# Optimization experiments

Measured on AMD Instinct MI355X. Metric: run time of the kernel, lower is better.

Reference implementation:

```python
import jax, jax.numpy as jnp
import numpy as np

D = 128      # dim_hidden
L = 8        # topological levels (level 0 = primary inputs)
M = 32768    # nodes per level
N = L * M
G = 5        # gate types: maj/not/and/or/xor -> 5 param sets
F = 2        # fan-in per gate node


def setup_inputs() -> dict:
    key = jax.random.key(0)
    ks = jax.random.split(key, 18)
    p = lambda k, sh: jax.random.normal(k, sh, jnp.float32) * 0.05
    return {
        's': jax.random.normal(ks[0], (N, D), jnp.float32),
        't': jax.random.normal(ks[1], (N, D), jnp.float32),
        'gate': jax.random.randint(ks[2], (N,), 0, G, jnp.int32),
        'fanin': jax.random.randint(ks[3], (L - 1, M, F), 0, M, jnp.int32),
        'hs_W': p(ks[4], (2 * D, D)), 'hs_b': p(ks[5], (D,)),
        'aggr_W1': p(ks[6], (G, 2 * D, D)), 'aggr_b1': p(ks[7], (G, D)),
        'aggr_W2': p(ks[8], (G, D, D)), 'aggr_b2': p(ks[9], (G, D)),
        'aggr_W3': p(ks[10], (G, D, D)), 'aggr_b3': p(ks[11], (G, D)),
        'gru_Wi': p(ks[12], (G, D, 3 * D)), 'gru_Wh': p(ks[13], (G, D, 3 * D)),
        'gru_bi': p(ks[14], (G, 3 * D)), 'gru_bh': p(ks[15], (G, 3 * D)),
    }


def _forward(s, t, gate, fanin, hs_W, hs_b, aggr_W1, aggr_b1, aggr_W2, aggr_b2,
             aggr_W3, aggr_b3, gru_Wi, gru_Wh, gru_bi, gru_bh):
    hs = jnp.concatenate([s, t], -1) @ hs_W + hs_b          # [N,D]
    hf = jnp.zeros((N, D), hs.dtype)                        # functional state, zero-init
    for lvl in range(1, L):                                 # level-synchronous sweep
        lo = lvl * M
        g_l = gate[lo:lo + M]                               # [M] gate type of dst nodes
        oh = jax.nn.one_hot(g_l, G, dtype=hs.dtype)         # [M,G] gate selector
        src = (lvl - 1) * M + fanin[lvl - 1]                # [M,F] global fan-in indices
        src_state = jnp.concatenate([hs[src], hf[src]], -1)  # [M,F,2D] node_state gather
        # per-gate-type edge MLP (TFMlpAggr): 3-layer MLP on source states, sum over fan-in
        h1 = jax.nn.relu(jnp.einsum('mfc,gcd->gmfd', src_state, aggr_W1) + aggr_b1[:, None, None, :])
        h2 = jax.nn.relu(jnp.einsum('gmfd,gde->gmfe', h1, aggr_W2) + aggr_b2[:, None, None, :])
        m = jnp.einsum('gmfe,gek->gmfk', h2, aggr_W3) + aggr_b3[:, None, None, :]
        msg = jnp.einsum('gmd,mg->md', m.sum(axis=2), oh)   # [M,D] select own gate's aggr
        # per-gate-type GRU update of hf (torch GRU math, seq_len=1)
        h = hf[lo:lo + M]                                   # [M,D]
        gi = jnp.einsum('md,gdk->gmk', msg, gru_Wi) + gru_bi[:, None, :]  # [G,M,3D]
        gh = jnp.einsum('md,gdk->gmk', h, gru_Wh) + gru_bh[:, None, :]
        r = jax.nn.sigmoid(gi[..., :D] + gh[..., :D])
        z = jax.nn.sigmoid(gi[..., D:2 * D] + gh[..., D:2 * D])
        n = jnp.tanh(gi[..., 2 * D:] + r * gh[..., 2 * D:])
        h_new = jnp.einsum('gmd,mg->md', (1.0 - z) * n + z * h[None], oh)
        hf = hf.at[lo:lo + M].set(h_new)                    # scatter-write back
    return hs, hf


def reference(s, t, gate, fanin, hs_W, hs_b, aggr_W1, aggr_b1, aggr_W2, aggr_b2,
              aggr_W3, aggr_b3, gru_Wi, gru_Wh, gru_bi, gru_bh):
    return _forward(s, t, gate, fanin, hs_W, hs_b, aggr_W1, aggr_b1, aggr_W2,
                    aggr_b2, aggr_W3, aggr_b3, gru_Wi, gru_Wh, gru_bi, gru_bh)
```

## Files before the change

kernel.cpp:

```cpp
#include <hip/hip_runtime.h>
#include <hip/hip_bf16.h>

#define DD 128
#define LL 8
#define MM 32768
#define NN (LL*MM)
#define GG 5
#define FF 2
#define SORT_STRIDE 33408

typedef __attribute__((ext_vector_type(8))) short short8;
typedef __attribute__((ext_vector_type(4))) short short4v;
typedef __attribute__((ext_vector_type(4))) float f32x4;

#define MFMA16(a,b,c) __builtin_amdgcn_mfma_f32_16x16x32_bf16((a),(b),(c),0,0,0)

__device__ __forceinline__ short f2bf(float x){
  __hip_bfloat16 h = __float2bfloat16(x);
  return *reinterpret_cast<short*>(&h);
}

__device__ __forceinline__ short8 pack8(f32x4 a, f32x4 b){
  short8 r;
  r[0]=f2bf(a[0]); r[1]=f2bf(a[1]); r[2]=f2bf(a[2]); r[3]=f2bf(a[3]);
  r[4]=f2bf(b[0]); r[5]=f2bf(b[1]); r[6]=f2bf(b[2]); r[7]=f2bf(b[3]);
  return r;
}

__global__ void prep_kernel(const float* __restrict__ hs_W, const float* __restrict__ W1,
                            const float* __restrict__ W2, const float* __restrict__ W3,
                            const float* __restrict__ Wi,
                            short* __restrict__ hsWt, short* __restrict__ W1t,
                            short* __restrict__ W2t, short* __restrict__ W3t,
                            short* __restrict__ Wit, int* __restrict__ cntcur)
{
  if (blockIdx.x == 0 && threadIdx.x < 70) cntcur[threadIdx.x] = 0;
  int u = blockIdx.x*256 + threadIdx.x;
  const float* src; short* dst; int ldw;
  if (u < 4096){
    int i=u, ct=i>>9, kc=(i>>6)&7, lane=i&63;
    src = hs_W + (size_t)(kc*32 + 8*(lane>>4))*128 + ct*16 + (lane&15);
    dst = hsWt + (size_t)i*8; ldw=128;
  } else if (u < 24576){
    int v=u-4096, g=v>>12, i=v&4095, ct=i>>9, kc=(i>>6)&7, lane=i&63;
    src = W1 + (size_t)g*32768 + (size_t)(kc*32 + 8*(lane>>4))*128 + ct*16 + (lane&15);
    dst = W1t + (size_t)g*32768 + i*8; ldw=128;
  } else if (u < 34816){
    int v=u-24576, g=v>>11, i=v&2047, ct=i>>8, kc=(i>>6)&3, lane=i&63;
    src = W2 + (size_t)g*16384 + (size_t)(kc*32 + 8*(lane>>4))*128 + ct*16 + (lane&15);
    dst = W2t + (size_t)g*16384 + i*8; ldw=128;
  } else if (u < 45056){
    int v=u-34816, g=v>>11, i=v&2047, ct=i>>8, kc=(i>>6)&3, lane=i&63;
    src = W3 + (size_t)g*16384 + (size_t)(kc*32 + 8*(lane>>4))*128 + ct*16 + (lane&15);
    dst = W3t + (size_t)g*16384 + i*8; ldw=128;
  } else {
    int v=u-45056, g=v/6144, i=v%6144, ct=i>>8, kc=(i>>6)&3, lane=i&63;
    src = Wi + (size_t)g*49152 + (size_t)(kc*32 + 8*(lane>>4))*384 + ct*16 + (lane&15);
    dst = Wit + (size_t)g*49152 + i*8; ldw=384;
  }
  short8 o;
#pragma unroll
  for (int j=0;j<8;++j) o[j] = f2bf(src[(size_t)j*ldw]);
  *(short8*)dst = o;
}

__global__ void count_kernel(const int* __restrict__ gate, int* __restrict__ cnt){
  __shared__ int lc[GG];
  const int li = blockIdx.x >> 7;
  const int m  = ((blockIdx.x & 127) << 8) + threadIdx.x;
  if (threadIdx.x < GG) lc[threadIdx.x] = 0;
  __syncthreads();
  int g = gate[(li+1)*MM + m];
  atomicAdd(&lc[g], 1);
  __syncthreads();
  if (threadIdx.x < GG && lc[threadIdx.x] > 0)
    atomicAdd(&cnt[li*GG + threadIdx.x], lc[threadIdx.x]);
}

__global__ void offs_kernel(const int* __restrict__ cnt, int* __restrict__ off,
                            int* __restrict__ pend, int* __restrict__ sorted){
  __shared__ int se[35], sp[35];
  const int tid = threadIdx.x;
  if (tid < LL-1){
    int l = tid, o = 0;
    for (int g = 0; g < GG; ++g){
      off[l*GG+g] = o;
      int c = cnt[l*GG+g];
      pend[l*GG+g] = o + c;
      se[l*GG+g] = o + c;
      o += ((c + 127) >> 7) << 7;
      sp[l*GG+g] = o;
    }
  }
  __syncthreads();
  for (int b = 0; b < 35; ++b){
    int l = b / GG;
    for (int i = se[b] + tid; i < sp[b]; i += 256)
      sorted[l*SORT_STRIDE + i] = -1;
  }
}

__global__ void scatter_kernel(const int* __restrict__ gate, const int* __restrict__ off,
                               int* __restrict__ cur, int* __restrict__ sorted){
  __shared__ int lc[GG];
  __shared__ int base[GG];
  const int li = blockIdx.x >> 7;
  const int m  = ((blockIdx.x & 127) << 8) + threadIdx.x;
  if (threadIdx.x < GG) lc[threadIdx.x] = 0;
  __syncthreads();
  int g = gate[(li+1)*MM + m];
  int p = atomicAdd(&lc[g], 1);
  __syncthreads();
  if (threadIdx.x < GG)
    base[threadIdx.x] = atomicAdd(&cur[li*GG + threadIdx.x], lc[threadIdx.x]);
  __syncthreads();
  sorted[li*SORT_STRIDE + off[li*GG+g] + base[g] + p] = m;
}

__global__ __launch_bounds__(512,4) void hs_kernel(
    const float* __restrict__ s, const float* __restrict__ t,
    const short* __restrict__ Wt, const float* __restrict__ b,
    float* __restrict__ hs, short* __restrict__ hs_sh,
    float* __restrict__ hf, short* __restrict__ hf_sh)
{
  __shared__ __align__(16) short Xs[32768];
  const int tid=threadIdx.x, lane=tid&63, w=tid>>6;
  const int l15=lane&15, lq=lane>>4;
  const int wr=w>>2, wc=w&3;
  const int row0 = blockIdx.x*128;

  {
    const int r = tid>>2, p = tid&3;
    const float* srow = s + (size_t)(row0+r)*DD;
    const float* trow = t + (size_t)(row0+r)*DD;
    const int rf = r>>4, rl = r&15;
#pragma unroll
    for (int i=0;i<8;++i){
      int u = p + 4*i;
      const float* pp = (u<16) ? (srow + 8*u) : (trow + 8*(u-16));
      short8 v = pack8(*(const f32x4*)pp, *(const f32x4*)(pp+4));
      *(short8*)(Xs + ((rf*8+(u>>2))*64 + (u&3)*16 + rl)*8) = v;
    }
  }

  if (row0 < MM){
    f32x4 zf4 = {0.f,0.f,0.f,0.f};
    short8 zs8 = {0,0,0,0,0,0,0,0};
    const size_t basei = (size_t)row0*DD;
    for (int i=tid; i<4096; i+=512) *(f32x4*)(hf + basei + i*4) = zf4;
    for (int i=tid; i<2048; i+=512) *(short8*)(hf_sh + basei + i*8) = zs8;
  }
  __syncthreads();

  f32x4 zf = {0.f,0.f,0.f,0.f};
  f32x4 acc[4][2];
#pragma unroll
  for (int rr=0;rr<4;++rr){ acc[rr][0]=zf; acc[rr][1]=zf; }

  const short* Ab = Wt + lane*8;
#pragma unroll
  for (int kc=0;kc<8;++kc){
    short8 a0 = *(const short8*)(Ab + (16*wc + kc)*512);
    short8 a1 = *(const short8*)(Ab + (16*wc + 8 + kc)*512);
#pragma unroll
    for (int rr=0;rr<4;++rr){
      short8 bx = *(const short8*)(Xs + (((4*wr+rr)*8 + kc)*64 + lane)*8);
      acc[rr][0] = MFMA16(a0, bx, acc[rr][0]);
      acc[rr][1] = MFMA16(a1, bx, acc[rr][1]);
    }
  }

  f32x4 bv0 = *(const f32x4*)(b + 32*wc + 4*lq);
  f32x4 bv1 = *(const f32x4*)(b + 32*wc + 16 + 4*lq);
#pragma unroll
  for (int rr=0;rr<4;++rr){
    int row = row0 + (4*wr+rr)*16 + l15;
#pragma unroll
    for (int q=0;q<2;++q){
      f32x4 bv = q ? bv1 : bv0;
      int col = 32*wc + 16*q + 4*lq;
      f32x4 o; short4v pk;
#pragma unroll
      for (int j=0;j<4;++j){ o[j] = acc[rr][q][j] + bv[j]; pk[j] = f2bf(o[j]); }
      *(f32x4*)(hs + (size_t)row*DD + col) = o;
      *(short4v*)(hs_sh + (size_t)row*DD + col) = pk;
    }
  }
}

__global__ __launch_bounds__(512,4) void level_kernel(
    int lvl, float* __restrict__ hfg,
    const short* __restrict__ hs_sh, short* __restrict__ hf_sh,
    const int* __restrict__ fanin,
    const short* __restrict__ W1t, const short* __restrict__ W2t,
    const short* __restrict__ W3t, const short* __restrict__ Wit,
    const float* __restrict__ b1, const float* __restrict__ b2,
    const float* __restrict__ b3, const float* __restrict__ bi,
    const float* __restrict__ bh,
    const int* __restrict__ off, const int* __restrict__ pend,
    const int* __restrict__ sorted)
{
  __shared__ __align__(16) short Xs[32768];
  __shared__ int nodebuf[64];
  __shared__ int srcbuf[128];
  __shared__ int ginfo;

  const int tid=threadIdx.x, lane=tid&63, w=tid>>6;
  const int l15=lane&15, lq=lane>>4;
  const int wr=w>>2, wc=w&3;
  const int li = lvl-1;
  const int pos0 = blockIdx.x*64;

  if (tid==0){
    int g=-1;
    for (int q=0;q<GG;++q)
      if (pos0>=off[li*GG+q] && pos0<pend[li*GG+q]){ g=q; break; }
    ginfo=g;
  }
  if (tid<64) nodebuf[tid] = sorted[li*SORT_STRIDE + pos0 + tid];
  if (tid<128){
    int mg = sorted[li*SORT_STRIDE + pos0 + (tid>>1)];
    srcbuf[tid] = (mg>=0) ? li*MM + fanin[((size_t)li*MM+mg)*FF + (tid&1)] : 0;
  }
  __syncthreads();
  const int g = ginfo;
  if (g<0) return;

  {
    const int r = tid>>2, p = tid&3;
    const int src = srcbuf[r];
    const short* hsrow = hs_sh + (size_t)src*DD;
    const short* hfrow = hf_sh + (size_t)src*DD;
    const int rf = r>>4, rl = r&15;
#pragma unroll
    for (int i=0;i<8;++i){
      int u = p + 4*i;
      short8 v = *(const short8*)((u<16) ? (hsrow + 8*u) : (hfrow + 8*(u-16)));
      *(short8*)(Xs + ((rf*8+(u>>2))*64 + (u&3)*16 + rl)*8) = v;
    }
  }
  __syncthreads();

  f32x4 zf = {0.f,0.f,0.f,0.f};

  f32x4 acc[4][2];
#pragma unroll
  for (int rr=0;rr<4;++rr){ acc[rr][0]=zf; acc[rr][1]=zf; }
  const short* A1 = W1t + (size_t)g*32768 + lane*8;
#pragma unroll
  for (int kc=0;kc<8;++kc){
    short8 a0 = *(const short8*)(A1 + (16*wc + kc)*512);
    short8 a1 = *(const short8*)(A1 + (16*wc + 8 + kc)*512);
#pragma unroll
    for (int rr=0;rr<4;++rr){
      short8 bx = *(const short8*)(Xs + (((4*wr+rr)*8 + kc)*64 + lane)*8);
      acc[rr][0] = MFMA16(a0, bx, acc[rr][0]);
      acc[rr][1] = MFMA16(a1, bx, acc[rr][1]);
    }
  }
  __syncthreads();
  {
    f32x4 bv0 = *(const f32x4*)(b1 + g*DD + 32*wc + 4*lq);
    f32x4 bv1 = *(const f32x4*)(b1 + g*DD + 32*wc + 16 + 4*lq);
#pragma unroll
    for (int rr=0;rr<4;++rr){
      int rf = 4*wr + rr;
#pragma unroll
      for (int q=0;q<2;++q){
        f32x4 bv = q ? bv1 : bv0;
        short4v pk;
#pragma unroll
        for (int j=0;j<4;++j) pk[j] = f2bf(fmaxf(acc[rr][q][j] + bv[j], 0.f));
        *(short4v*)(Xs + ((rf*4 + wc)*64 + (2*q + (lq>>1))*16 + l15)*8 + 4*(lq&1)) = pk;
      }
    }
  }
  __syncthreads();

  f32x4 acc2[4][2];
#pragma unroll
  for (int rr=0;rr<4;++rr){ acc2[rr][0]=zf; acc2[rr][1]=zf; }
  const short* A2 = W2t + (size_t)g*16384 + lane*8;
#pragma unroll
  for (int kc=0;kc<4;++kc){
    short8 a0 = *(const short8*)(A2 + (8*wc + kc)*512);
    short8 a1 = *(const short8*)(A2 + (8*wc + 4 + kc)*512);
#pragma unroll
    for (int rr=0;rr<4;++rr){
      short8 bx = *(const short8*)(Xs + (((4*wr+rr)*4 + kc)*64 + lane)*8);
      acc2[rr][0] = MFMA16(a0, bx, acc2[rr][0]);
      acc2[rr][1] = MFMA16(a1, bx, acc2[rr][1]);
    }
  }
  {
    f32x4 bv0 = *(const f32x4*)(b2 + g*DD + 32*wc + 4*lq);
    f32x4 bv1 = *(const f32x4*)(b2 + g*DD + 32*wc + 16 + 4*lq);
#pragma unroll
    for (int rr=0;rr<4;++rr){
      int rf = 4*wr + rr;
#pragma unroll
      for (int q=0;q<2;++q){
        f32x4 bv = q ? bv1 : bv0;
        short4v pk;
#pragma unroll
        for (int j=0;j<4;++j) pk[j] = f2bf(fmaxf(acc2[rr][q][j] + bv[j], 0.f));
        *(short4v*)(Xs + 16384 + ((rf*4 + wc)*64 + (2*q + (lq>>1))*16 + l15)*8 + 4*(lq&1)) = pk;
      }
    }
  }
  __syncthreads();

  f32x4 acc3[4][2];
#pragma unroll
  for (int rr=0;rr<4;++rr){ acc3[rr][0]=zf; acc3[rr][1]=zf; }
  const short* A3 = W3t + (size_t)g*16384 + lane*8;
#pragma unroll
  for (int kc=0;kc<4;++kc){
    short8 a0 = *(const short8*)(A3 + (8*wc + kc)*512);
    short8 a1 = *(const short8*)(A3 + (8*wc + 4 + kc)*512);
#pragma unroll
    for (int rr=0;rr<4;++rr){
      short8 bx = *(const short8*)(Xs + 16384 + (((4*wr+rr)*4 + kc)*64 + lane)*8);
      acc3[rr][0] = MFMA16(a0, bx, acc3[rr][0]);
      acc3[rr][1] = MFMA16(a1, bx, acc3[rr][1]);
    }
  }
  {
    f32x4 bv0 = *(const f32x4*)(b3 + g*DD + 32*wc + 4*lq);
    f32x4 bv1 = *(const f32x4*)(b3 + g*DD + 32*wc + 16 + 4*lq);
#pragma unroll
    for (int rr=0;rr<4;++rr){
#pragma unroll
      for (int q=0;q<2;++q){
        f32x4 bv = q ? bv1 : bv0;
        f32x4 mv;
#pragma unroll
        for (int j=0;j<4;++j){
          float v = acc3[rr][q][j];
          mv[j] = v + __shfl_xor(v, 1) + 2.f*bv[j];
        }
        if ((l15 & 1) == 0){
          int n = (4*wr+rr)*8 + (l15>>1);
          short4v pk;
#pragma unroll
          for (int j=0;j<4;++j) pk[j] = f2bf(mv[j]);
          *(short4v*)(Xs + (((n>>4)*4 + wc)*64 + (2*q + (lq>>1))*16 + (n&15))*8 + 4*(lq&1)) = pk;
        }
      }
    }
  }
  __syncthreads();

  f32x4 gr[4], gz[4], gn[4];
#pragma unroll
  for (int rfm=0;rfm<4;++rfm){ gr[rfm]=zf; gz[rfm]=zf; gn[rfm]=zf; }
  const short* AW = Wit + (size_t)g*49152 + lane*8;
#pragma unroll
  for (int kc=0;kc<4;++kc){
    short8 aR = *(const short8*)(AW + ((w)*4 + kc)*512);
    short8 aZ = *(const short8*)(AW + ((8+w)*4 + kc)*512);
    short8 aN = *(const short8*)(AW + ((16+w)*4 + kc)*512);
#pragma unroll
    for (int rfm=0;rfm<4;++rfm){
      short8 bm = *(const short8*)(Xs + ((rfm*4 + kc)*64 + lane)*8);
      gr[rfm] = MFMA16(aR, bm, gr[rfm]);
      gz[rfm] = MFMA16(aZ, bm, gz[rfm]);
      gn[rfm] = MFMA16(aN, bm, gn[rfm]);
    }
  }

  const int lo = lvl*MM;
  f32x4 biR = *(const f32x4*)(bi + g*384 + 16*w + 4*lq);
  f32x4 biZ = *(const f32x4*)(bi + g*384 + 128 + 16*w + 4*lq);
  f32x4 biN = *(const f32x4*)(bi + g*384 + 256 + 16*w + 4*lq);
  f32x4 bhR = *(const f32x4*)(bh + g*384 + 16*w + 4*lq);
  f32x4 bhZ = *(const f32x4*)(bh + g*384 + 128 + 16*w + 4*lq);
  f32x4 bhN = *(const f32x4*)(bh + g*384 + 256 + 16*w + 4*lq);
#pragma unroll
  for (int rfm=0;rfm<4;++rfm){
    int m = nodebuf[rfm*16 + l15];
    if (m < 0) continue;
    f32x4 o; short4v pk;
#pragma unroll
    for (int j=0;j<4;++j){
      float xr = gr[rfm][j] + biR[j] + bhR[j];
      float xz = gz[rfm][j] + biZ[j] + bhZ[j];
      float r_ = 1.f/(1.f + __expf(-xr));
      float z_ = 1.f/(1.f + __expf(-xz));
      float xn = gn[rfm][j] + biN[j] + r_*bhN[j];
      float n_ = 2.f/(1.f + __expf(-2.f*xn)) - 1.f;
      o[j] = (1.f - z_)*n_;
      pk[j] = f2bf(o[j]);
    }
    int col = 16*w + 4*lq;
    *(f32x4*)(hfg + (size_t)(lo + m)*DD + col) = o;
    *(short4v*)(hf_sh + (size_t)(lo + m)*DD + col) = pk;
  }
}

extern "C" void kernel_launch(void* const* d_in, const int* in_sizes, int n_in,
                              void* d_out, int out_size, void* d_ws, size_t ws_size,
                              hipStream_t stream)
{
  const float* s    = (const float*)d_in[0];
  const float* t    = (const float*)d_in[1];
  const int*   gate = (const int*)d_in[2];
  const int*   fanin= (const int*)d_in[3];
  const float* hs_W = (const float*)d_in[4];
  const float* hs_b = (const float*)d_in[5];
  const float* W1   = (const float*)d_in[6];
  const float* b1   = (const float*)d_in[7];
  const float* W2   = (const float*)d_in[8];
  const float* b2   = (const float*)d_in[9];
  const float* W3   = (const float*)d_in[10];
  const float* b3   = (const float*)d_in[11];
  const float* Wi   = (const float*)d_in[12];
  const float* bi   = (const float*)d_in[14];
  const float* bh   = (const float*)d_in[15];

  float* hs = (float*)d_out;
  float* hf = hs + (size_t)NN*DD;

  int* cnt    = (int*)d_ws;
  int* cur    = cnt + 35;
  int* off    = cnt + 70;
  int* pendv  = cnt + 105;
  int* sorted = cnt + 256;

  short* wbase = (short*)((char*)d_ws + (1<<20));
  short* hsWt = wbase;
  short* W1t  = wbase + 32768;
  short* W2t  = wbase + 196608;
  short* W3t  = wbase + 278528;
  short* Wit  = wbase + 360448;

  short* hs_sh = (short*)((char*)d_ws + (size_t)(8<<20));
  short* hf_sh = hs_sh + (size_t)NN*DD;

  prep_kernel<<<296, 256, 0, stream>>>(hs_W, W1, W2, W3, Wi,
                                       hsWt, W1t, W2t, W3t, Wit, cnt);
  count_kernel<<<896, 256, 0, stream>>>(gate, cnt);
  offs_kernel<<<1, 256, 0, stream>>>(cnt, off, pendv, sorted);
  scatter_kernel<<<896, 256, 0, stream>>>(gate, off, cur, sorted);
  hs_kernel<<<NN/128, 512, 0, stream>>>(s, t, hsWt, hs_b, hs, hs_sh, hf, hf_sh);
  for (int lvl = 1; lvl < LL; ++lvl){
    level_kernel<<<SORT_STRIDE/64, 512, 0, stream>>>(lvl, hf,
        hs_sh, hf_sh, fanin, W1t, W2t, W3t, Wit,
        b1, b2, b3, bi, bh, off, pendv, sorted);
  }
}
```

Measured before the change: 414.1 us.

## Halve level-kernel tile to 32 nodes with 256 threads and finer gate padding

Each level-kernel block now handles 32 destination nodes with 4 waves instead of 64 nodes with 8 waves. Shared memory is halved and the per-wave MFMA mapping is rearranged so each wave owns a 32-column slice for every GEMM, including the GRU stage. Per-gate bucket padding drops from 128 to 32, which wastes fewer padded rows across the 5 gate types and gives more blocks. In exchange, each weight fragment loaded from global memory is reused over fewer rows, so weight traffic per node roughly doubles.

```diff
diff --git a/kernel.cpp b/kernel.cpp
--- a/kernel.cpp
+++ b/kernel.cpp
@@ -88,7 +88,7 @@
       int c = cnt[l*GG+g];
       pend[l*GG+g] = o + c;
       se[l*GG+g] = o + c;
-      o += ((c + 127) >> 7) << 7;
+      o += ((c + 31) >> 5) << 5;
       sp[l*GG+g] = o;
     }
   }
@@ -188,7 +188,7 @@
   }
 }
 
-__global__ __launch_bounds__(512,4) void level_kernel(
+__global__ __launch_bounds__(256,4) void level_kernel(
     int lvl, float* __restrict__ hfg,
     const short* __restrict__ hs_sh, short* __restrict__ hf_sh,
     const int* __restrict__ fanin,
@@ -200,16 +200,15 @@
     const int* __restrict__ off, const int* __restrict__ pend,
     const int* __restrict__ sorted)
 {
-  __shared__ __align__(16) short Xs[32768];
-  __shared__ int nodebuf[64];
-  __shared__ int srcbuf[128];
+  __shared__ __align__(16) short Xs[16384];
+  __shared__ int nodebuf[32];
+  __shared__ int srcbuf[64];
   __shared__ int ginfo;
 
   const int tid=threadIdx.x, lane=tid&63, w=tid>>6;
   const int l15=lane&15, lq=lane>>4;
-  const int wr=w>>2, wc=w&3;
   const int li = lvl-1;
-  const int pos0 = blockIdx.x*64;
+  const int pos0 = blockIdx.x*32;
 
   if (tid==0){
     int g=-1;
@@ -217,8 +216,8 @@
       if (pos0>=off[li*GG+q] && pos0<pend[li*GG+q]){ g=q; break; }
     ginfo=g;
   }
-  if (tid<64) nodebuf[tid] = sorted[li*SORT_STRIDE + pos0 + tid];
-  if (tid<128){
+  if (tid<32) nodebuf[tid] = sorted[li*SORT_STRIDE + pos0 + tid];
+  if (tid<64){
     int mg = sorted[li*SORT_STRIDE + pos0 + (tid>>1)];
     srcbuf[tid] = (mg>=0) ? li*MM + fanin[((size_t)li*MM+mg)*FF + (tid&1)] : 0;
   }
@@ -249,29 +248,28 @@
   const short* A1 = W1t + (size_t)g*32768 + lane*8;
 #pragma unroll
   for (int kc=0;kc<8;++kc){
-    short8 a0 = *(const short8*)(A1 + (16*wc + kc)*512);
-    short8 a1 = *(const short8*)(A1 + (16*wc + 8 + kc)*512);
-#pragma unroll
-    for (int rr=0;rr<4;++rr){
-      short8 bx = *(const short8*)(Xs + (((4*wr+rr)*8 + kc)*64 + lane)*8);
+    short8 a0 = *(const short8*)(A1 + (16*w + kc)*512);
+    short8 a1 = *(const short8*)(A1 + (16*w + 8 + kc)*512);
+#pragma unroll
+    for (int rr=0;rr<4;++rr){
+      short8 bx = *(const short8*)(Xs + ((rr*8 + kc)*64 + lane)*8);
       acc[rr][0] = MFMA16(a0, bx, acc[rr][0]);
       acc[rr][1] = MFMA16(a1, bx, acc[rr][1]);
     }
   }
   __syncthreads();
   {
-    f32x4 bv0 = *(const f32x4*)(b1 + g*DD + 32*wc + 4*lq);
-    f32x4 bv1 = *(const f32x4*)(b1 + g*DD + 32*wc + 16 + 4*lq);
-#pragma unroll
-    for (int rr=0;rr<4;++rr){
-      int rf = 4*wr + rr;
+    f32x4 bv0 = *(const f32x4*)(b1 + g*DD + 32*w + 4*lq);
+    f32x4 bv1 = *(const f32x4*)(b1 + g*DD + 32*w + 16 + 4*lq);
+#pragma unroll
+    for (int rr=0;rr<4;++rr){
 #pragma unroll
       for (int q=0;q<2;++q){
         f32x4 bv = q ? bv1 : bv0;
         short4v pk;
 #pragma unroll
         for (int j=0;j<4;++j) pk[j] = f2bf(fmaxf(acc[rr][q][j] + bv[j], 0.f));
-        *(short4v*)(Xs + ((rf*4 + wc)*64 + (2*q + (lq>>1))*16 + l15)*8 + 4*(lq&1)) = pk;
+        *(short4v*)(Xs + ((rr*4 + w)*64 + (2*q + (lq>>1))*16 + l15)*8 + 4*(lq&1)) = pk;
       }
     }
   }
@@ -283,28 +281,27 @@
   const short* A2 = W2t + (size_t)g*16384 + lane*8;
 #pragma unroll
   for (int kc=0;kc<4;++kc){
-    short8 a0 = *(const short8*)(A2 + (8*wc + kc)*512);
-    short8 a1 = *(const short8*)(A2 + (8*wc + 4 + kc)*512);
-#pragma unroll
-    for (int rr=0;rr<4;++rr){
-      short8 bx = *(const short8*)(Xs + (((4*wr+rr)*4 + kc)*64 + lane)*8);
+    short8 a0 = *(const short8*)(A2 + (8*w + kc)*512);
+    short8 a1 = *(const short8*)(A2 + (8*w + 4 + kc)*512);
+#pragma unroll
+    for (int rr=0;rr<4;++rr){
+      short8 bx = *(const short8*)(Xs + ((rr*4 + kc)*64 + lane)*8);
       acc2[rr][0] = MFMA16(a0, bx, acc2[rr][0]);
       acc2[rr][1] = MFMA16(a1, bx, acc2[rr][1]);
     }
   }
   {
-    f32x4 bv0 = *(const f32x4*)(b2 + g*DD + 32*wc + 4*lq);
-    f32x4 bv1 = *(const f32x4*)(b2 + g*DD + 32*wc + 16 + 4*lq);
-#pragma unroll
-    for (int rr=0;rr<4;++rr){
-      int rf = 4*wr + rr;
+    f32x4 bv0 = *(const f32x4*)(b2 + g*DD + 32*w + 4*lq);
+    f32x4 bv1 = *(const f32x4*)(b2 + g*DD + 32*w + 16 + 4*lq);
+#pragma unroll
+    for (int rr=0;rr<4;++rr){
 #pragma unroll
       for (int q=0;q<2;++q){
         f32x4 bv = q ? bv1 : bv0;
         short4v pk;
 #pragma unroll
         for (int j=0;j<4;++j) pk[j] = f2bf(fmaxf(acc2[rr][q][j] + bv[j], 0.f));
-        *(short4v*)(Xs + 16384 + ((rf*4 + wc)*64 + (2*q + (lq>>1))*16 + l15)*8 + 4*(lq&1)) = pk;
+        *(short4v*)(Xs + 8192 + ((rr*4 + w)*64 + (2*q + (lq>>1))*16 + l15)*8 + 4*(lq&1)) = pk;
       }
     }
   }
@@ -316,18 +313,18 @@
   const short* A3 = W3t + (size_t)g*16384 + lane*8;
 #pragma unroll
   for (int kc=0;kc<4;++kc){
-    short8 a0 = *(const short8*)(A3 + (8*wc + kc)*512);
-    short8 a1 = *(const short8*)(A3 + (8*wc + 4 + kc)*512);
-#pragma unroll
-    for (int rr=0;rr<4;++rr){
-      short8 bx = *(const short8*)(Xs + 16384 + (((4*wr+rr)*4 + kc)*64 + lane)*8);
+    short8 a0 = *(const short8*)(A3 + (8*w + kc)*512);
+    short8 a1 = *(const short8*)(A3 + (8*w + 4 + kc)*512);
+#pragma unroll
+    for (int rr=0;rr<4;++rr){
+      short8 bx = *(const short8*)(Xs + 8192 + ((rr*4 + kc)*64 + lane)*8);
       acc3[rr][0] = MFMA16(a0, bx, acc3[rr][0]);
       acc3[rr][1] = MFMA16(a1, bx, acc3[rr][1]);
     }
   }
   {
-    f32x4 bv0 = *(const f32x4*)(b3 + g*DD + 32*wc + 4*lq);
-    f32x4 bv1 = *(const f32x4*)(b3 + g*DD + 32*wc + 16 + 4*lq);
+    f32x4 bv0 = *(const f32x4*)(b3 + g*DD + 32*w + 4*lq);
+    f32x4 bv1 = *(const f32x4*)(b3 + g*DD + 32*w + 16 + 4*lq);
 #pragma unroll
     for (int rr=0;rr<4;++rr){
 #pragma unroll
@@ -340,61 +337,72 @@
           mv[j] = v + __shfl_xor(v, 1) + 2.f*bv[j];
         }
         if ((l15 & 1) == 0){
-          int n = (4*wr+rr)*8 + (l15>>1);
+          int n = rr*8 + (l15>>1);
           short4v pk;
 #pragma unroll
           for (int j=0;j<4;++j) pk[j] = f2bf(mv[j]);
-          *(short4v*)(Xs + (((n>>4)*4 + wc)*64 + (2*q + (lq>>1))*16 + (n&15))*8 + 4*(lq&1)) = pk;
+          *(short4v*)(Xs + (((n>>4)*4 + w)*64 + (2*q + (lq>>1))*16 + (n&15))*8 + 4*(lq&1)) = pk;
         }
       }
     }
   }
   __syncthreads();
 
-  f32x4 gr[4], gz[4], gn[4];
-#pragma unroll
-  for (int rfm=0;rfm<4;++rfm){ gr[rfm]=zf; gz[rfm]=zf; gn[rfm]=zf; }
+  f32x4 gr[2][2], gz[2][2], gn[2][2];
+#pragma unroll
+  for (int rfm=0;rfm<2;++rfm)
+#pragma unroll
+    for (int q=0;q<2;++q){ gr[rfm][q]=zf; gz[rfm][q]=zf; gn[rfm][q]=zf; }
   const short* AW = Wit + (size_t)g*49152 + lane*8;
 #pragma unroll
   for (int kc=0;kc<4;++kc){
-    short8 aR = *(const short8*)(AW + ((w)*4 + kc)*512);
-    short8 aZ = *(const short8*)(AW + ((8+w)*4 + kc)*512);
-    short8 aN = *(const short8*)(AW + ((16+w)*4 + kc)*512);
-#pragma unroll
-    for (int rfm=0;rfm<4;++rfm){
+    short8 aR0 = *(const short8*)(AW + (8*w + kc)*512);
+    short8 aR1 = *(const short8*)(AW + (8*w + 4 + kc)*512);
+    short8 aZ0 = *(const short8*)(AW + 16384 + (8*w + kc)*512);
+    short8 aZ1 = *(const short8*)(AW + 16384 + (8*w + 4 + kc)*512);
+    short8 aN0 = *(const short8*)(AW + 32768 + (8*w + kc)*512);
+    short8 aN1 = *(const short8*)(AW + 32768 + (8*w + 4 + kc)*512);
+#pragma unroll
+    for (int rfm=0;rfm<2;++rfm){
       short8 bm = *(const short8*)(Xs + ((rfm*4 + kc)*64 + lane)*8);
-      gr[rfm] = MFMA16(aR, bm, gr[rfm]);
-      gz[rfm] = MFMA16(aZ, bm, gz[rfm]);
-      gn[rfm] = MFMA16(aN, bm, gn[rfm]);
+      gr[rfm][0] = MFMA16(aR0, bm, gr[rfm][0]);
+      gr[rfm][1] = MFMA16(aR1, bm, gr[rfm][1]);
+      gz[rfm][0] = MFMA16(aZ0, bm, gz[rfm][0]);
+      gz[rfm][1] = MFMA16(aZ1, bm, gz[rfm][1]);
+      gn[rfm][0] = MFMA16(aN0, bm, gn[rfm][0]);
+      gn[rfm][1] = MFMA16(aN1, bm, gn[rfm][1]);
     }
   }
 
   const int lo = lvl*MM;
-  f32x4 biR = *(const f32x4*)(bi + g*384 + 16*w + 4*lq);
-  f32x4 biZ = *(const f32x4*)(bi + g*384 + 128 + 16*w + 4*lq);
-  f32x4 biN = *(const f32x4*)(bi + g*384 + 256 + 16*w + 4*lq);
-  f32x4 bhR = *(const f32x4*)(bh + g*384 + 16*w + 4*lq);
-  f32x4 bhZ = *(const f32x4*)(bh + g*384 + 128 + 16*w + 4*lq);
-  f32x4 bhN = *(const f32x4*)(bh + g*384 + 256 + 16*w + 4*lq);
-#pragma unroll
-  for (int rfm=0;rfm<4;++rfm){
-    int m = nodebuf[rfm*16 + l15];
-    if (m < 0) continue;
-    f32x4 o; short4v pk;
-#pragma unroll
-    for (int j=0;j<4;++j){
-      float xr = gr[rfm][j] + biR[j] + bhR[j];
-      float xz = gz[rfm][j] + biZ[j] + bhZ[j];
-      float r_ = 1.f/(1.f + __expf(-xr));
-      float z_ = 1.f/(1.f + __expf(-xz));
-      float xn = gn[rfm][j] + biN[j] + r_*bhN[j];
-      float n_ = 2.f/(1.f + __expf(-2.f*xn)) - 1.f;
-      o[j] = (1.f - z_)*n_;
-      pk[j] = f2bf(o[j]);
-    }
-    int col = 16*w + 4*lq;
-    *(f32x4*)(hfg + (size_t)(lo + m)*DD + col) = o;
-    *(short4v*)(hf_sh + (size_t)(lo + m)*DD + col) = pk;
+#pragma unroll
+  for (int q=0;q<2;++q){
+    int col = 32*w + 16*q + 4*lq;
+    f32x4 biR = *(const f32x4*)(bi + g*384 + col);
+    f32x4 biZ = *(const f32x4*)(bi + g*384 + 128 + col);
+    f32x4 biN = *(const f32x4*)(bi + g*384 + 256 + col);
+    f32x4 bhR = *(const f32x4*)(bh + g*384 + col);
+    f32x4 bhZ = *(const f32x4*)(bh + g*384 + 128 + col);
+    f32x4 bhN = *(const f32x4*)(bh + g*384 + 256 + col);
+#pragma unroll
+    for (int rfm=0;rfm<2;++rfm){
+      int m = nodebuf[rfm*16 + l15];
+      if (m < 0) continue;
+      f32x4 o; short4v pk;
+#pragma unroll
+      for (int j=0;j<4;++j){
+        float xr = gr[rfm][q][j] + biR[j] + bhR[j];
+        float xz = gz[rfm][q][j] + biZ[j] + bhZ[j];
+        float r_ = 1.f/(1.f + __expf(-xr));
+        float z_ = 1.f/(1.f + __expf(-xz));
+        float xn = gn[rfm][q][j] + biN[j] + r_*bhN[j];
+        float n_ = 2.f/(1.f + __expf(-2.f*xn)) - 1.f;
+        o[j] = (1.f - z_)*n_;
+        pk[j] = f2bf(o[j]);
+      }
+      *(f32x4*)(hfg + (size_t)(lo + m)*DD + col) = o;
+      *(short4v*)(hf_sh + (size_t)(lo + m)*DD + col) = pk;
+    }
   }
 }
 
@@ -444,7 +452,7 @@
   scatter_kernel<<<896, 256, 0, stream>>>(gate, off, cur, sorted);
   hs_kernel<<<NN/128, 512, 0, stream>>>(s, t, hsWt, hs_b, hs, hs_sh, hf, hf_sh);
   for (int lvl = 1; lvl < LL; ++lvl){
-    level_kernel<<<SORT_STRIDE/64, 512, 0, stream>>>(lvl, hf,
+    level_kernel<<<SORT_STRIDE/32, 256, 0, stream>>>(lvl, hf,
         hs_sh, hf_sh, fanin, W1t, W2t, W3t, Wit,
         b1, b2, b3, bi, bh, off, pendv, sorted);
   }
```

After: 397.2 us. -4.1%, faster.
